# Performance work log

Hardware: AMD Instinct MI355X
Metric: run time of the kernel (lower is better)

The kernel has to match this reference:

```python
import jax, jax.numpy as jnp
import numpy as np


def setup_inputs() -> dict:
    key = jax.random.key(0)
    ks = jax.random.split(key, 9)
    B, C, H, W = 4, 256, 128, 128
    d = C // 8
    x = jax.random.normal(ks[0], (B, C, H, W), jnp.float32)
    wq = jax.random.normal(ks[1], (d, C), jnp.float32) * 0.05
    bq = jax.random.normal(ks[2], (d,), jnp.float32) * 0.05
    wk = jax.random.normal(ks[3], (d, C), jnp.float32) * 0.05
    bk = jax.random.normal(ks[4], (d,), jnp.float32) * 0.05
    wv = jax.random.normal(ks[5], (d, C), jnp.float32) * 0.05
    bv = jax.random.normal(ks[6], (d,), jnp.float32) * 0.05
    wp = jax.random.normal(ks[7], (C, d, 3, 3), jnp.float32) * 0.05
    gamma = jax.random.normal(ks[8], (1,), jnp.float32)
    return dict(x=x, wq=wq, bq=bq, wk=wk, bk=bk, wv=wv, bv=bv, wp=wp, gamma=gamma)


def reference(x, wq, bq, wk, bk, wv, bv, wp, gamma):
    B, C, H, W = x.shape
    d = wq.shape[0]  # C // 8
    N = H * W
    # 1x1 convs expressed as channel matmuls
    q = jnp.einsum('bchw,dc->bdhw', x, wq) + bq[None, :, None, None]
    k = jnp.einsum('bchw,dc->bdhw', x, wk) + bk[None, :, None, None]
    v = jnp.einsum('bchw,dc->bdhw', x, wv) + bv[None, :, None, None]
    Q = q.reshape(B, d, N)
    K = k.reshape(B, d, N)
    V = v.reshape(B, d, N)
    # channel-channel energy: [B, d, d]
    energy = jnp.einsum('bdn,ben->bde', Q, K)
    energy_new = jnp.max(energy, axis=-1, keepdims=True) - energy
    attention = jax.nn.softmax(energy_new, axis=-1)
    out = jnp.einsum('bde,ben->bdn', attention, V).reshape(B, d, H, W)
    # 3x3 conv (no bias) + exact GELU
    out = jax.lax.conv_general_dilated(
        out, wp, window_strides=(1, 1), padding='SAME',
        dimension_numbers=('NCHW', 'OIHW', 'NCHW'))
    out = jax.nn.gelu(out, approximate=False)
    return gamma[0] * out + x
```

## Files before the change

### kernel.cpp

```cpp
#include <hip/hip_runtime.h>
#include <hip/hip_bf16.h>
#include <math.h>

#define BB 4
#define CC 256
#define HH 128
#define WW 128
#define NN (HH*WW)
#define DD 32

#define AOT_CI   44
#define AOT_ROWE (130*AOT_CI)
#define AOT_IMGE (130*AOT_ROWE)
#define AOT_BYTES ((size_t)BB*AOT_IMGE*2)
#define AOT_ALLOC (AOT_BYTES + 1024)

#define WT_BYTES (9*256*AOT_CI*2)

#define PATCH_SZ 45760
#define WSLAB    22528
#define CONV_LDS (PATCH_SZ + 2*WSLAB)
#define EPI_PITCH 260

#define ASWZ_BYTES 98304
#define QKVP 260
#define QKV_LDS 131584

typedef __attribute__((ext_vector_type(8)))  short bf16x8;
typedef __attribute__((ext_vector_type(4)))  float f32x4;
typedef __attribute__((ext_vector_type(16))) float f32x16;

__device__ inline void async_copy16(void* lds, const void* g) {
    __builtin_amdgcn_global_load_lds(
        (const __attribute__((address_space(1))) unsigned int*)g,
        (__attribute__((address_space(3))) unsigned int*)lds, 16, 0, 0);
}

__device__ inline unsigned short f2bf(float f) {
    __hip_bfloat16 h = __float2bfloat16(f);
    return *reinterpret_cast<unsigned short*>(&h);
}

__device__ inline void split2(float v, unsigned short& h, unsigned short& l) {
    __hip_bfloat16 hb = __float2bfloat16(v);
    float r = v - __bfloat162float(hb);
    __hip_bfloat16 lb = __float2bfloat16(r);
    h = *reinterpret_cast<unsigned short*>(&hb);
    l = *reinterpret_cast<unsigned short*>(&lb);
}

__device__ inline unsigned int packsplit(float v) {
    unsigned int fb = __float_as_uint(v);
    unsigned int hb = fb & 0xFFFF0000u;
    float r = v - __uint_as_float(hb);
    unsigned int lb = __float_as_uint(r) >> 16;
    return (hb >> 16) | (lb << 16);
}

__device__ inline bf16x8 ld_frag8(const char* p) {
    union { bf16x8 v; short4 h[2]; } u;
    u.h[0] = *(const short4*)(p);
    u.h[1] = *(const short4*)(p + 8);
    return u.v;
}

__device__ inline float gelu_fast(float v) {
    float a = fabsf(v) * 0.70710678118654752f;
    float t = __fdividef(1.0f, fmaf(0.3275911f, a, 1.0f));
    float p = t * fmaf(t, fmaf(t, fmaf(t, fmaf(t, 1.061405429f, -1.453152027f),
                                       1.421413741f), -0.284496736f), 0.254829592f);
    float e = 1.0f - p * __expf(-a * a);
    float erfv = (v < 0.0f) ? -e : e;
    return 0.5f * v * (1.0f + erfv);
}

__global__ __launch_bounds__(256) void prep_kernel(
    const float* __restrict__ wp, unsigned short* __restrict__ Wt,
    const float* __restrict__ wq, const float* __restrict__ wk,
    const float* __restrict__ wv, unsigned short* __restrict__ Aswz,
    unsigned short* __restrict__ AOT)
{
    const int blk = blockIdx.x;
    if (blk < 288) {
        int i = blk*256 + threadIdx.x;
        int kk = i / (256*32);
        int r  = i % (256*32);
        int co = r >> 5, ci = r & 31;
        float v = wp[((size_t)co*32 + ci)*9 + kk];
        Wt[((size_t)kk*256 + co)*AOT_CI + ci] = f2bf(v);
    } else if (blk < 480) {
        int i = (blk-288)*256 + threadIdx.x;
        int j    = i & 7;
        int lane = (i >> 3) & 63;
        int q9   = i >> 9;
        int cf   = q9 % 3;
        int t    = q9 / 3;
        int hl   = t & 1;
        int s    = t >> 1;
        int row  = cf*32 + (lane & 31);
        int c    = s*16 + (lane >> 5)*8 + j;
        float w  = (row < 32) ? wq[row*256 + c]
                 : (row < 64) ? wk[(row-32)*256 + c]
                              : wv[(row-64)*256 + c];
        unsigned short h, l;
        split2(w, h, l);
        Aswz[i] = hl ? l : h;
    } else {
        int idx = (blk-480)*256 + threadIdx.x;
        if (idx < BB*22704) {
            int b = idx / 22704;
            int r = idx % 22704;
            size_t off;
            if (r < 11440) {
                int row = (r < 5720) ? 0 : 129;
                int e   = (r < 5720) ? r : r - 5720;
                off = (size_t)b*AOT_IMGE + (size_t)row*AOT_ROWE + e;
            } else {
                int r2 = r - 11440;
                int rr = r2 / 88 + 1;
                int w2 = r2 % 88;
                int col = (w2 < 44) ? 0 : 129;
                int ci  = (w2 < 44) ? w2 : w2 - 44;
                off = (size_t)b*AOT_IMGE + (size_t)rr*AOT_ROWE
                    + (size_t)col*AOT_CI + ci;
            }
            AOT[off] = 0;
        }
    }
}

__global__ __launch_bounds__(512, 1) void qkv_mfma_kernel(
    const float* __restrict__ x, const unsigned short* __restrict__ Aswz,
    const float* __restrict__ bq, const float* __restrict__ bk,
    const float* __restrict__ bv,
    float* __restrict__ Vout, float* __restrict__ Ep)
{
    __shared__ __align__(16) char lds[QKV_LDS];
    const int b    = blockIdx.y;
    const int s    = blockIdx.x;
    const int n0   = s * 256;
    const int tid  = threadIdx.x;
    const int w    = tid >> 6;
    const int lane = tid & 63;
    const int l31  = lane & 31;
    const int lh   = lane >> 5;
    const int chl  = lane >> 3;
    const int nq   = lane & 7;

    for (int i = tid; i < 6144; i += 512)
        async_copy16(lds + i*16, (const char*)Aswz + i*16);
    float* biasL = (float*)(lds + 131072);
    if (tid < 96)
        biasL[tid] = (tid < 32) ? bq[tid] : (tid < 64) ? bk[tid-32] : bv[tid-64];

    char* mybuf = lds + 98304 + w*4096;
    const float* xq4 = x + (size_t)b*CC*NN + n0 + 32*w + nq*4;

    f32x16 acc0 = {0}, acc1 = {0}, acc2 = {0};

    float4 sa0, sb0, sa1, sb1, sa2, sb2;
    #define LOADX(VA, VB, R) do { \
        VA = *(const float4*)(xq4 + (size_t)((R)*16 + chl    )*NN); \
        VB = *(const float4*)(xq4 + (size_t)((R)*16 + 8 + chl)*NN); } while (0)
    #define PACKW(R, VA, VB) do { \
        unsigned int* bp = (unsigned int*)(mybuf + ((R) & 1)*2048); \
        uint4 ua, ub; \
        ua.x = packsplit((VA).x); ua.y = packsplit((VA).y); \
        ua.z = packsplit((VA).z); ua.w = packsplit((VA).w); \
        ub.x = packsplit((VB).x); ub.y = packsplit((VB).y); \
        ub.z = packsplit((VB).z); ub.w = packsplit((VB).w); \
        *(uint4*)(bp + (chl    )*32 + nq*4) = ua; \
        *(uint4*)(bp + (8 + chl)*32 + nq*4) = ub; } while (0)

    LOADX(sa0, sb0, 0);
    LOADX(sa1, sb1, 1);
    LOADX(sa2, sb2, 2);
    PACKW(0, sa0, sb0);
    __syncthreads();

    #pragma unroll
    for (int r = 0; r < 16; ++r) {
        if (r + 3 < 16) {
            if ((r+3) % 3 == 0)      LOADX(sa0, sb0, r+3);
            else if ((r+3) % 3 == 1) LOADX(sa1, sb1, r+3);
            else                     LOADX(sa2, sb2, r+3);
        }
        {
            const unsigned int* bufc = (const unsigned int*)(mybuf + (r & 1)*2048);
            unsigned int u[8];
            #pragma unroll
            for (int j = 0; j < 8; ++j)
                u[j] = bufc[(lh*8 + j)*32 + l31];
            union { bf16x8 v; unsigned int d[4]; } B1, B2;
            #pragma unroll
            for (int dq = 0; dq < 4; ++dq) {
                B1.d[dq] = (u[2*dq] & 0xFFFFu) | (u[2*dq+1] << 16);
                B2.d[dq] = (u[2*dq] >> 16)     | (u[2*dq+1] & 0xFFFF0000u);
            }
            #pragma unroll
            for (int cf = 0; cf < 3; ++cf) {
                bf16x8 ah = *(const bf16x8*)(lds + (((r*6 +     cf)*64) + lane)*16);
                bf16x8 al = *(const bf16x8*)(lds + (((r*6 + 3 + cf)*64) + lane)*16);
                f32x16* ac = (cf == 0) ? &acc0 : (cf == 1) ? &acc1 : &acc2;
                *ac = __builtin_amdgcn_mfma_f32_32x32x16_bf16(ah, B1.v, *ac, 0, 0, 0);
                *ac = __builtin_amdgcn_mfma_f32_32x32x16_bf16(ah, B2.v, *ac, 0, 0, 0);
                *ac = __builtin_amdgcn_mfma_f32_32x32x16_bf16(al, B1.v, *ac, 0, 0, 0);
                *ac = __builtin_amdgcn_mfma_f32_32x32x16_bf16(al, B2.v, *ac, 0, 0, 0);
            }
        }
        if (r + 1 < 16) {
            if ((r+1) % 3 == 0)      PACKW(r+1, sa0, sb0);
            else if ((r+1) % 3 == 1) PACKW(r+1, sa1, sb1);
            else                     PACKW(r+1, sa2, sb2);
        }
    }
    #undef LOADX
    #undef PACKW

    __syncthreads();
    float* qk = (float*)lds;
    #pragma unroll
    for (int r = 0; r < 16; ++r) {
        const int rsub = (r & 3) + 8*(r >> 2) + 4*lh;
        const int col  = 32*w + l31;
        qk[rsub*QKVP + col]      = acc0[r] + biasL[rsub];
        qk[(32+rsub)*QKVP + col] = acc1[r] + biasL[32 + rsub];
        Vout[((size_t)b*DD + rsub)*NN + n0 + col] = acc2[r] + biasL[64 + rsub];
    }
    __syncthreads();

    const int d  = tid >> 4;
    const int e2 = tid & 15;
    const float* qrow = qk + d*QKVP;
    float s0 = 0.f, s1 = 0.f;
    for (int n4 = 0; n4 < 256; n4 += 4) {
        float4 qv = *(const float4*)(qrow + n4);
        float4 ka = *(const float4*)(qk + (32 + e2)*QKVP + n4);
        float4 kb = *(const float4*)(qk + (48 + e2)*QKVP + n4);
        s0 += qv.x*ka.x + qv.y*ka.y + qv.z*ka.z + qv.w*ka.w;
        s1 += qv.x*kb.x + qv.y*kb.y + qv.z*kb.z + qv.w*kb.w;
    }
    float* ep = Ep + ((size_t)s*BB + b)*1024;
    ep[d*32 + e2]      = s0;
    ep[d*32 + e2 + 16] = s1;
}

__global__ __launch_bounds__(1024) void softmax_kernel(
    const float* __restrict__ Ep, float* __restrict__ attT)
{
    const int b = blockIdx.x;
    const int e = threadIdx.x, d = threadIdx.y;
    float s = 0.f;
    #pragma unroll 8
    for (int p = 0; p < 64; ++p)
        s += Ep[((size_t)p * BB + b) * (DD * DD) + d * DD + e];
    float nv = -s;
    float m = nv;
    for (int off = 16; off > 0; off >>= 1) m = fmaxf(m, __shfl_xor(m, off, 32));
    float pe = expf(nv - m);
    float su = pe;
    for (int off = 16; off > 0; off >>= 1) su += __shfl_xor(su, off, 32);
    attT[(size_t)b * (DD * DD) + e * DD + d] = pe / su;
}

__global__ __launch_bounds__(256) void pv_kernel(
    const float* __restrict__ V, const float* __restrict__ attT,
    unsigned short* __restrict__ AOT)
{
    __shared__ float Vs[DD][128];
    __shared__ float at4[DD][DD];
    const int b  = blockIdx.y;
    const int n0 = blockIdx.x * 128;
    const int tid = threadIdx.x;
    for (int i = tid; i < 1024; i += 256) {
        int r = i >> 5, c4 = i & 31;
        *(float4*)&Vs[r][c4*4] =
            *(const float4*)(V + ((size_t)b*DD + r)*NN + n0 + c4*4);
    }
    for (int i = tid; i < 1024; i += 256)
        at4[i >> 5][i & 31] = attT[(size_t)b*1024 + i];
    __syncthreads();
    const int nl = tid & 127;
    const int dg = tid >> 7;
    float acc[16];
    #pragma unroll
    for (int k = 0; k < 16; ++k) acc[k] = 0.f;
    #pragma unroll 4
    for (int e = 0; e < DD; ++e) {
        float v = Vs[e][nl];
        const float4* ar = (const float4*)&at4[e][dg*16];
        #pragma unroll
        for (int q = 0; q < 4; ++q) {
            float4 a = ar[q];
            acc[4*q+0] += a.x * v; acc[4*q+1] += a.y * v;
            acc[4*q+2] += a.z * v; acc[4*q+3] += a.w * v;
        }
    }
    const int n = n0 + nl;
    const int h = n >> 7, ww = n & 127;
    unsigned short* dst = AOT + (size_t)b*AOT_IMGE + (size_t)(h+1)*AOT_ROWE
                              + (size_t)(ww+1)*AOT_CI + dg*16;
    #pragma unroll
    for (int q = 0; q < 4; ++q) {
        ushort4 u;
        u.x = f2bf(acc[4*q+0]); u.y = f2bf(acc[4*q+1]);
        u.z = f2bf(acc[4*q+2]); u.w = f2bf(acc[4*q+3]);
        *(ushort4*)(dst + 4*q) = u;
    }
}

__global__ __launch_bounds__(512, 1) void conv_kernel(
    const unsigned short* __restrict__ AOT, const unsigned short* __restrict__ Wt,
    const float* __restrict__ gammap, const float* __restrict__ x,
    float* __restrict__ out)
{
    __shared__ __align__(16) char lds[CONV_LDS];
    const int b   = blockIdx.y;
    const int h0  = blockIdx.x * 2;
    const int tid = threadIdx.x;
    const int wid = tid >> 6;
    const int lane = tid & 63;
    const int l15 = lane & 15;
    const int lj  = lane >> 4;
    const int wn  = wid & 1;
    const int wc  = wid >> 1;

    const char* psrc = (const char*)(AOT + (size_t)b*AOT_IMGE + (size_t)h0*AOT_ROWE);
    for (int i = tid; i < PATCH_SZ/16; i += 512)
        async_copy16(lds + i*16, psrc + i*16);
    for (int i = tid; i < WSLAB/16; i += 512)
        async_copy16(lds + PATCH_SZ + i*16, (const char*)Wt + i*16);
    __syncthreads();

    f32x4 acc[4][8];
    #pragma unroll
    for (int cf = 0; cf < 4; ++cf)
        #pragma unroll
        for (int nf = 0; nf < 8; ++nf)
            acc[cf][nf] = (f32x4){0.f, 0.f, 0.f, 0.f};

    for (int kk = 0; kk < 9; ++kk) {
        if (kk < 8) {
            const char* wsrc = (const char*)Wt + (size_t)(kk+1)*WSLAB;
            char* wdst = lds + PATCH_SZ + ((kk+1)&1)*WSLAB;
            for (int i = tid; i < WSLAB/16; i += 512)
                async_copy16(wdst + i*16, wsrc + i*16);
        }
        const int kh = kk / 3, kw = kk % 3;
        const char* wbase = lds + PATCH_SZ + (kk&1)*WSLAB;
        bf16x8 af[4];
        #pragma unroll
        for (int cf = 0; cf < 4; ++cf)
            af[cf] = ld_frag8(wbase + (wc*64 + cf*16 + l15)*88 + lj*16);
        #pragma unroll
        for (int nf = 0; nf < 8; ++nf) {
            const int cell = (wn + kh)*130 + nf*16 + l15 + kw;
            const bf16x8 bfr = ld_frag8(lds + cell*88 + lj*16);
            #pragma unroll
            for (int cf = 0; cf < 4; ++cf)
                acc[cf][nf] = __builtin_amdgcn_mfma_f32_16x16x32_bf16(
                    af[cf], bfr, acc[cf][nf], 0, 0, 0);
        }
        __syncthreads();
    }

    const float g0 = gammap[0];
    float* lf = (float*)lds;
    for (int k = 0; k < 4; ++k) {
        if (wc == k) {
            #pragma unroll
            for (int cf = 0; cf < 4; ++cf) {
                const int rl = cf*16 + 4*lj;
                #pragma unroll
                for (int nf = 0; nf < 8; ++nf) {
                    const int col = wn*128 + nf*16 + l15;
                    #pragma unroll
                    for (int j = 0; j < 4; ++j)
                        lf[(rl + j)*EPI_PITCH + col] = acc[cf][nf][j];
                }
            }
        }
        __syncthreads();
        #pragma unroll
        for (int it = 0; it < 8; ++it) {
            const int idx = tid + it*512;
            const int row = idx >> 6, c4 = idx & 63;
            const int co  = k*64 + row;
            const size_t g = ((size_t)b*CC + co)*NN + (size_t)h0*WW + c4*4;
            float4 v  = *(const float4*)(lf + row*EPI_PITCH + c4*4);
            float4 xv = *(const float4*)(x + g);
            float4 o;
            o.x = g0*gelu_fast(v.x) + xv.x;
            o.y = g0*gelu_fast(v.y) + xv.y;
            o.z = g0*gelu_fast(v.z) + xv.z;
            o.w = g0*gelu_fast(v.w) + xv.w;
            *(float4*)(out + g) = o;
        }
        __syncthreads();
    }
}

extern "C" void kernel_launch(void* const* d_in, const int* in_sizes, int n_in,
                              void* d_out, int out_size, void* d_ws, size_t ws_size,
                              hipStream_t stream)
{
    const float* x  = (const float*)d_in[0];
    const float* wq = (const float*)d_in[1];
    const float* bq = (const float*)d_in[2];
    const float* wk = (const float*)d_in[3];
    const float* bk = (const float*)d_in[4];
    const float* wv = (const float*)d_in[5];
    const float* bv = (const float*)d_in[6];
    const float* wp = (const float*)d_in[7];
    const float* gm = (const float*)d_in[8];
    float* out = (float*)d_out;

    float* Vbuf = out;

    char* ws = (char*)d_ws;
    unsigned short* AOT  = (unsigned short*)ws;
    unsigned short* Wt   = (unsigned short*)(ws + AOT_ALLOC);
    unsigned short* Aswz = (unsigned short*)(ws + AOT_ALLOC + WT_BYTES);
    float* Ep  = (float*)(ws + AOT_ALLOC + WT_BYTES + ASWZ_BYTES);
    float* ATT = Ep + (size_t)64*BB*1024;

    prep_kernel    <<<dim3(835), 256, 0, stream>>>(wp, Wt, wq, wk, wv, Aswz, AOT);
    qkv_mfma_kernel<<<dim3(64, BB), 512, 0, stream>>>(x, Aswz, bq, bk, bv, Vbuf, Ep);
    softmax_kernel <<<dim3(BB), dim3(32, 32), 0, stream>>>(Ep, ATT);
    pv_kernel      <<<dim3(128, BB), 256, 0, stream>>>(Vbuf, ATT, AOT);
    conv_kernel    <<<dim3(64, BB), 512, 0, stream>>>(AOT, Wt, gm, x, out);
}
```

Measured before the change: 79.88 us.

## Fuse softmax into PV kernel and shrink conv blocks to one row

Result: faster. 75.75 us, median of 2 (-5.2%).

```diff
diff --git a/kernel.cpp b/kernel.cpp
--- a/kernel.cpp
+++ b/kernel.cpp
@@ -17,10 +17,10 @@
 
 #define WT_BYTES (9*256*AOT_CI*2)
 
-#define PATCH_SZ 45760
+#define PATCH1   34320
 #define WSLAB    22528
-#define CONV_LDS (PATCH_SZ + 2*WSLAB)
-#define EPI_PITCH 260
+#define CONV_LDS1 (PATCH1 + 2*WSLAB)
+#define EPI1_PITCH 132
 
 #define ASWZ_BYTES 98304
 #define QKVP 260
@@ -245,63 +245,69 @@
     ep[d*32 + e2 + 16] = s1;
 }
 
-__global__ __launch_bounds__(1024) void softmax_kernel(
-    const float* __restrict__ Ep, float* __restrict__ attT)
-{
-    const int b = blockIdx.x;
-    const int e = threadIdx.x, d = threadIdx.y;
-    float s = 0.f;
-    #pragma unroll 8
-    for (int p = 0; p < 64; ++p)
-        s += Ep[((size_t)p * BB + b) * (DD * DD) + d * DD + e];
-    float nv = -s;
-    float m = nv;
-    for (int off = 16; off > 0; off >>= 1) m = fmaxf(m, __shfl_xor(m, off, 32));
-    float pe = expf(nv - m);
-    float su = pe;
-    for (int off = 16; off > 0; off >>= 1) su += __shfl_xor(su, off, 32);
-    attT[(size_t)b * (DD * DD) + e * DD + d] = pe / su;
-}
-
 __global__ __launch_bounds__(256) void pv_kernel(
-    const float* __restrict__ V, const float* __restrict__ attT,
+    const float* __restrict__ V, const float* __restrict__ Ep,
     unsigned short* __restrict__ AOT)
 {
-    __shared__ float Vs[DD][128];
+    __shared__ float Vs[DD][256];
     __shared__ float at4[DD][DD];
     const int b  = blockIdx.y;
-    const int n0 = blockIdx.x * 128;
+    const int n0 = blockIdx.x * 256;
     const int tid = threadIdx.x;
-    for (int i = tid; i < 1024; i += 256) {
-        int r = i >> 5, c4 = i & 31;
+    for (int i = tid; i < 2048; i += 256) {
+        int r = i >> 6, c4 = i & 63;
         *(float4*)&Vs[r][c4*4] =
             *(const float4*)(V + ((size_t)b*DD + r)*NN + n0 + c4*4);
     }
-    for (int i = tid; i < 1024; i += 256)
-        at4[i >> 5][i & 31] = attT[(size_t)b*1024 + i];
+    {
+        const int d  = tid >> 3;
+        const int eb = (tid & 7) * 4;
+        float4 sum = {0.f, 0.f, 0.f, 0.f};
+        #pragma unroll 8
+        for (int p = 0; p < 64; ++p) {
+            float4 v = *(const float4*)(Ep + ((size_t)p*BB + b)*1024 + d*32 + eb);
+            sum.x += v.x; sum.y += v.y; sum.z += v.z; sum.w += v.w;
+        }
+        float nv0 = -sum.x, nv1 = -sum.y, nv2 = -sum.z, nv3 = -sum.w;
+        float m = fmaxf(fmaxf(nv0, nv1), fmaxf(nv2, nv3));
+        m = fmaxf(m, __shfl_xor(m, 4, 8));
+        m = fmaxf(m, __shfl_xor(m, 2, 8));
+        m = fmaxf(m, __shfl_xor(m, 1, 8));
+        float p0 = expf(nv0 - m), p1 = expf(nv1 - m);
+        float p2 = expf(nv2 - m), p3 = expf(nv3 - m);
+        float su = p0 + p1 + p2 + p3;
+        su += __shfl_xor(su, 4, 8);
+        su += __shfl_xor(su, 2, 8);
+        su += __shfl_xor(su, 1, 8);
+        const float inv = 1.0f / su;
+        at4[eb + 0][d] = p0 * inv;
+        at4[eb + 1][d] = p1 * inv;
+        at4[eb + 2][d] = p2 * inv;
+        at4[eb + 3][d] = p3 * inv;
+    }
     __syncthreads();
-    const int nl = tid & 127;
-    const int dg = tid >> 7;
-    float acc[16];
+
+    const int t = tid;
+    float acc[DD];
     #pragma unroll
-    for (int k = 0; k < 16; ++k) acc[k] = 0.f;
+    for (int k = 0; k < DD; ++k) acc[k] = 0.f;
     #pragma unroll 4
     for (int e = 0; e < DD; ++e) {
-        float v = Vs[e][nl];
-        const float4* ar = (const float4*)&at4[e][dg*16];
+        float v = Vs[e][t];
+        const float4* ar = (const float4*)at4[e];
         #pragma unroll
-        for (int q = 0; q < 4; ++q) {
-            float4 a = ar[q];
-            acc[4*q+0] += a.x * v; acc[4*q+1] += a.y * v;
-            acc[4*q+2] += a.z * v; acc[4*q+3] += a.w * v;
-        }
-    }
-    const int n = n0 + nl;
+        for (int dq = 0; dq < 8; ++dq) {
+            float4 a = ar[dq];
+            acc[4*dq+0] += a.x * v; acc[4*dq+1] += a.y * v;
+            acc[4*dq+2] += a.z * v; acc[4*dq+3] += a.w * v;
+        }
+    }
+    const int n = n0 + t;
     const int h = n >> 7, ww = n & 127;
     unsigned short* dst = AOT + (size_t)b*AOT_IMGE + (size_t)(h+1)*AOT_ROWE
-                              + (size_t)(ww+1)*AOT_CI + dg*16;
+                              + (size_t)(ww+1)*AOT_CI;
     #pragma unroll
-    for (int q = 0; q < 4; ++q) {
+    for (int q = 0; q < 8; ++q) {
         ushort4 u;
         u.x = f2bf(acc[4*q+0]); u.y = f2bf(acc[4*q+1]);
         u.z = f2bf(acc[4*q+2]); u.w = f2bf(acc[4*q+3]);
@@ -309,27 +315,25 @@
     }
 }
 
-__global__ __launch_bounds__(512, 1) void conv_kernel(
+__global__ __launch_bounds__(256, 2) void conv_kernel(
     const unsigned short* __restrict__ AOT, const unsigned short* __restrict__ Wt,
     const float* __restrict__ gammap, const float* __restrict__ x,
     float* __restrict__ out)
 {
-    __shared__ __align__(16) char lds[CONV_LDS];
+    __shared__ __align__(16) char lds[CONV_LDS1];
     const int b   = blockIdx.y;
-    const int h0  = blockIdx.x * 2;
+    const int h   = blockIdx.x;
     const int tid = threadIdx.x;
     const int wid = tid >> 6;
     const int lane = tid & 63;
     const int l15 = lane & 15;
     const int lj  = lane >> 4;
-    const int wn  = wid & 1;
-    const int wc  = wid >> 1;
-
-    const char* psrc = (const char*)(AOT + (size_t)b*AOT_IMGE + (size_t)h0*AOT_ROWE);
-    for (int i = tid; i < PATCH_SZ/16; i += 512)
+
+    const char* psrc = (const char*)(AOT + (size_t)b*AOT_IMGE + (size_t)h*AOT_ROWE);
+    for (int i = tid; i < PATCH1/16; i += 256)
         async_copy16(lds + i*16, psrc + i*16);
-    for (int i = tid; i < WSLAB/16; i += 512)
-        async_copy16(lds + PATCH_SZ + i*16, (const char*)Wt + i*16);
+    for (int i = tid; i < WSLAB/16; i += 256)
+        async_copy16(lds + PATCH1 + i*16, (const char*)Wt + i*16);
     __syncthreads();
 
     f32x4 acc[4][8];
@@ -342,19 +346,19 @@
     for (int kk = 0; kk < 9; ++kk) {
         if (kk < 8) {
             const char* wsrc = (const char*)Wt + (size_t)(kk+1)*WSLAB;
-            char* wdst = lds + PATCH_SZ + ((kk+1)&1)*WSLAB;
-            for (int i = tid; i < WSLAB/16; i += 512)
+            char* wdst = lds + PATCH1 + ((kk+1)&1)*WSLAB;
+            for (int i = tid; i < WSLAB/16; i += 256)
                 async_copy16(wdst + i*16, wsrc + i*16);
         }
         const int kh = kk / 3, kw = kk % 3;
-        const char* wbase = lds + PATCH_SZ + (kk&1)*WSLAB;
+        const char* wbase = lds + PATCH1 + (kk&1)*WSLAB;
         bf16x8 af[4];
         #pragma unroll
         for (int cf = 0; cf < 4; ++cf)
-            af[cf] = ld_frag8(wbase + (wc*64 + cf*16 + l15)*88 + lj*16);
+            af[cf] = ld_frag8(wbase + (wid*64 + cf*16 + l15)*88 + lj*16);
         #pragma unroll
         for (int nf = 0; nf < 8; ++nf) {
-            const int cell = (wn + kh)*130 + nf*16 + l15 + kw;
+            const int cell = kh*130 + nf*16 + l15 + kw;
             const bf16x8 bfr = ld_frag8(lds + cell*88 + lj*16);
             #pragma unroll
             for (int cf = 0; cf < 4; ++cf)
@@ -367,27 +371,27 @@
     const float g0 = gammap[0];
     float* lf = (float*)lds;
     for (int k = 0; k < 4; ++k) {
-        if (wc == k) {
+        if (wid == k) {
             #pragma unroll
             for (int cf = 0; cf < 4; ++cf) {
                 const int rl = cf*16 + 4*lj;
                 #pragma unroll
                 for (int nf = 0; nf < 8; ++nf) {
-                    const int col = wn*128 + nf*16 + l15;
+                    const int col = nf*16 + l15;
                     #pragma unroll
                     for (int j = 0; j < 4; ++j)
-                        lf[(rl + j)*EPI_PITCH + col] = acc[cf][nf][j];
+                        lf[(rl + j)*EPI1_PITCH + col] = acc[cf][nf][j];
                 }
             }
         }
         __syncthreads();
         #pragma unroll
         for (int it = 0; it < 8; ++it) {
-            const int idx = tid + it*512;
-            const int row = idx >> 6, c4 = idx & 63;
+            const int idx = tid + it*256;
+            const int row = idx >> 5, c4 = idx & 31;
             const int co  = k*64 + row;
-            const size_t g = ((size_t)b*CC + co)*NN + (size_t)h0*WW + c4*4;
-            float4 v  = *(const float4*)(lf + row*EPI_PITCH + c4*4);
+            const size_t g = ((size_t)b*CC + co)*NN + (size_t)h*WW + c4*4;
+            float4 v  = *(const float4*)(lf + row*EPI1_PITCH + c4*4);
             float4 xv = *(const float4*)(x + g);
             float4 o;
             o.x = g0*gelu_fast(v.x) + xv.x;
@@ -422,11 +426,9 @@
     unsigned short* Wt   = (unsigned short*)(ws + AOT_ALLOC);
     unsigned short* Aswz = (unsigned short*)(ws + AOT_ALLOC + WT_BYTES);
     float* Ep  = (float*)(ws + AOT_ALLOC + WT_BYTES + ASWZ_BYTES);
-    float* ATT = Ep + (size_t)64*BB*1024;
 
     prep_kernel    <<<dim3(835), 256, 0, stream>>>(wp, Wt, wq, wk, wv, Aswz, AOT);
     qkv_mfma_kernel<<<dim3(64, BB), 512, 0, stream>>>(x, Aswz, bq, bk, bv, Vbuf, Ep);
-    softmax_kernel <<<dim3(BB), dim3(32, 32), 0, stream>>>(Ep, ATT);
-    pv_kernel      <<<dim3(128, BB), 256, 0, stream>>>(Vbuf, ATT, AOT);
-    conv_kernel    <<<dim3(64, BB), 512, 0, stream>>>(AOT, Wt, gm, x, out);
-}
+    pv_kernel      <<<dim3(64, BB), 256, 0, stream>>>(Vbuf, Ep, AOT);
+    conv_kernel    <<<dim3(HH, BB), 256, 0, stream>>>(AOT, Wt, gm, x, out);
+}
```
